# Performance work log

Measured on AMD Instinct MI355X. Metric: run time of the kernel, lower is better.

## Reference

```python
import jax, jax.numpy as jnp
import numpy as np

N = 20000; P = 3; L_LP = 10; L_NS = 20; D = 128; OUT = 2; E = 640000; V_LP = 5000; V_NS = 10000


def _gru(x, lengths, W_ih, W_hh, b_ih, b_hh):
    # x: [B, T, Din]; returns last valid hidden state per sequence (pack_padded semantics)
    T = x.shape[1]
    xp = jnp.einsum('btd,gd->btg', x, W_ih) + b_ih  # [B, T, 3H]
    h0 = jnp.zeros((x.shape[0], W_hh.shape[1]), x.dtype)

    def step(h, inp):
        xpt, t = inp
        hp = h @ W_hh.T + b_hh
        xr, xz, xn = jnp.split(xpt, 3, axis=-1)
        hr, hz, hn = jnp.split(hp, 3, axis=-1)
        r = jax.nn.sigmoid(xr + hr)
        z = jax.nn.sigmoid(xz + hz)
        nn_ = jnp.tanh(xn + r * hn)
        h_new = (1.0 - z) * nn_ + z * h
        h = jnp.where((t < lengths)[:, None], h_new, h)
        return h, None

    hT, _ = jax.lax.scan(step, h0, (jnp.swapaxes(xp, 0, 1), jnp.arange(T)))
    return hT


def _gcn(x, src, dst, w, W, b, n):
    # PyG GCNConv: add self-loops (weight 1), symmetric normalization by in-degree
    loops = jnp.arange(n)
    s = jnp.concatenate([src, loops])
    d = jnp.concatenate([dst, loops])
    ww = jnp.concatenate([w, jnp.ones((n,), w.dtype)])
    deg = jax.ops.segment_sum(ww, d, num_segments=n)
    dinv = jnp.where(deg > 0, 1.0 / jnp.sqrt(deg), 0.0)
    norm = dinv[s] * ww * dinv[d]
    xw = x @ W.T
    return jax.ops.segment_sum(norm[:, None] * xw[s], d, num_segments=n) + b


def _lnorm(x, g, b):
    m = jnp.mean(x, axis=-1, keepdims=True)
    v = jnp.var(x, axis=-1, keepdims=True)
    return (x - m) / jnp.sqrt(v + 1e-5) * g + b


def _forward(x_ref, x_def, x_pdt, edge_weight, lp_emb, ns_emb, lp_Wih, lp_Whh, lp_bih, lp_bhh, ns_Wih, ns_Whh, ns_bih, ns_bhh, lp_fc_W, lp_fc_b, all_fc_W, all_fc_b, conv1_W, conv1_b, conv2_W, conv2_b, conv3_W, conv3_b, ln1_g, ln1_b, ln2_g, ln2_b, mp1_W, mp1_b, mp2_W, mp2_b, idx_lp, x_lp_length, idx_ns, x_ns_length, edge_index):
    n = idx_ns.shape[0]
    # long-path GRU encodings, one GRU run per path slot (vmapped over P)
    xl = lp_emb[idx_lp]  # [N, P, L_LP, D]
    gru_lp = lambda seq, lens: _gru(seq, lens, lp_Wih, lp_Whh, lp_bih, lp_bhh)
    h_lp = jax.vmap(gru_lp, in_axes=(1, 1))(xl, x_lp_length)  # [P, N, D]
    # torch.cat(h_list).view(N, D*P): row-major reshape of [P, N, D]
    x_lp = h_lp.reshape(n, P * D) @ lp_fc_W.T + lp_fc_b
    # natural-sequence GRU encoding
    x_ns = _gru(ns_emb[idx_ns], x_ns_length, ns_Wih, ns_Whh, ns_bih, ns_bhh)  # [N, D]
    # torch.cat(dim=0).view(N, 5D): faithful row-major reshape of [5N, D]
    x = jnp.concatenate([x_pdt, x_ref, x_def, x_lp, x_ns], axis=0).reshape(n, 5 * D)
    x = x @ all_fc_W.T + all_fc_b
    src, dst = edge_index[0], edge_index[1]
    convs = [(conv1_W, conv1_b), (conv2_W, conv2_b), (conv3_W, conv3_b)]
    lns = [(ln1_g, ln1_b), (ln2_g, ln2_b)]
    emb = x
    for i in range(3):
        x = _gcn(x, src, dst, edge_weight, convs[i][0], convs[i][1], n)
        emb = x
        x = jax.nn.relu(x)
        # dropout p=0.25 omitted (eval mode)
        if i < 2:
            x = _lnorm(x, lns[i][0], lns[i][1])
    x = x @ mp1_W.T + mp1_b
    x = x @ mp2_W.T + mp2_b
    return emb, jax.nn.log_softmax(x, axis=1)


def setup_inputs() -> dict:
    ks = jax.random.split(jax.random.key(0), 40)
    f32 = jnp.float32
    nrm = lambda k, sh, s: jax.random.normal(k, sh, f32) * s
    inp = {}
    inp['idx_lp'] = jax.random.randint(ks[0], (N, P, L_LP), 0, V_LP)
    inp['x_lp_length'] = jax.random.randint(ks[1], (N, P), 1, L_LP + 1)
    inp['idx_ns'] = jax.random.randint(ks[2], (N, L_NS), 0, V_NS)
    inp['x_ns_length'] = jax.random.randint(ks[3], (N,), 1, L_NS + 1)
    inp['x_ref'] = nrm(ks[4], (N, D), 1.0)
    inp['x_def'] = nrm(ks[5], (N, D), 1.0)
    inp['x_pdt'] = nrm(ks[6], (N, D), 1.0)
    inp['edge_index'] = jax.random.randint(ks[7], (2, E), 0, N)
    inp['edge_weight'] = jax.random.uniform(ks[8], (E,), f32)
    inp['lp_emb'] = nrm(ks[9], (V_LP, D), 0.5)
    inp['ns_emb'] = nrm(ks[10], (V_NS, D), 0.5)
    s = 0.08
    inp['lp_Wih'] = nrm(ks[11], (3 * D, D), s)
    inp['lp_Whh'] = nrm(ks[12], (3 * D, D), s)
    inp['lp_bih'] = nrm(ks[13], (3 * D,), s)
    inp['lp_bhh'] = nrm(ks[14], (3 * D,), s)
    inp['ns_Wih'] = nrm(ks[15], (3 * D, D), s)
    inp['ns_Whh'] = nrm(ks[16], (3 * D, D), s)
    inp['ns_bih'] = nrm(ks[17], (3 * D,), s)
    inp['ns_bhh'] = nrm(ks[18], (3 * D,), s)
    inp['lp_fc_W'] = nrm(ks[19], (D, P * D), 0.05)
    inp['lp_fc_b'] = nrm(ks[20], (D,), 0.05)
    inp['all_fc_W'] = nrm(ks[21], (D, 5 * D), 0.05)
    inp['all_fc_b'] = nrm(ks[22], (D,), 0.05)
    inp['conv1_W'] = nrm(ks[23], (D, D), 0.08)
    inp['conv1_b'] = nrm(ks[24], (D,), 0.05)
    inp['conv2_W'] = nrm(ks[25], (D, D), 0.08)
    inp['conv2_b'] = nrm(ks[26], (D,), 0.05)
    inp['conv3_W'] = nrm(ks[27], (D, D), 0.08)
    inp['conv3_b'] = nrm(ks[28], (D,), 0.05)
    inp['ln1_g'] = jnp.ones((D,), f32)
    inp['ln1_b'] = jnp.zeros((D,), f32)
    inp['ln2_g'] = jnp.ones((D,), f32)
    inp['ln2_b'] = jnp.zeros((D,), f32)
    inp['mp1_W'] = nrm(ks[29], (D, D), 0.08)
    inp['mp1_b'] = nrm(ks[30], (D,), 0.05)
    inp['mp2_W'] = nrm(ks[31], (OUT, D), 0.08)
    inp['mp2_b'] = nrm(ks[32], (OUT,), 0.05)
    return inp


def reference(idx_lp, x_lp_length, idx_ns, x_ns_length, x_ref, x_def, x_pdt, edge_index, edge_weight, lp_emb, ns_emb, lp_Wih, lp_Whh, lp_bih, lp_bhh, ns_Wih, ns_Whh, ns_bih, ns_bhh, lp_fc_W, lp_fc_b, all_fc_W, all_fc_b, conv1_W, conv1_b, conv2_W, conv2_b, conv3_W, conv3_b, ln1_g, ln1_b, ln2_g, ln2_b, mp1_W, mp1_b, mp2_W, mp2_b):
    return _forward(x_ref, x_def, x_pdt, edge_weight, lp_emb, ns_emb, lp_Wih, lp_Whh, lp_bih, lp_bhh, ns_Wih, ns_Whh, ns_bih, ns_bhh, lp_fc_W, lp_fc_b, all_fc_W, all_fc_b, conv1_W, conv1_b, conv2_W, conv2_b, conv3_W, conv3_b, ln1_g, ln1_b, ln2_g, ln2_b, mp1_W, mp1_b, mp2_W, mp2_b, idx_lp, x_lp_length, idx_ns, x_ns_length, edge_index)
```

## Files before the change

### kernel.cpp

```cpp
#include <hip/hip_runtime.h>
#include <math.h>

typedef unsigned short u16;
typedef short bf16x4 __attribute__((ext_vector_type(4)));
typedef short bf16x8 __attribute__((ext_vector_type(8)));
typedef float f32x16 __attribute__((ext_vector_type(16)));

#define NN 20000
#define PP 3
#define TLP 10
#define TNS 20
#define DD 128
#define EE 640000

__device__ __forceinline__ float bf2f(u16 u) {
  union { unsigned u; float f; } v; v.u = ((unsigned)u) << 16; return v.f;
}
__device__ __forceinline__ u16 f2bf(float f) {
  union { float f; unsigned u; } v; v.f = f;
  unsigned r = v.u + 0x7fffu + ((v.u >> 16) & 1u);
  return (u16)(r >> 16);
}
__device__ __forceinline__ short f2bf_hw(float f) {
  __bf16 b = (__bf16)f;
  return (short)__builtin_bit_cast(unsigned short, b);
}
__device__ __forceinline__ float loadf(const void* p, size_t i, int isf) {
  return isf ? ((const float*)p)[i] : bf2f(((const u16*)p)[i]);
}
__device__ __forceinline__ float fex2(float x) { return __builtin_amdgcn_exp2f(x); }
__device__ __forceinline__ float frcp(float x) { return __builtin_amdgcn_rcpf(x); }
__device__ __forceinline__ unsigned cvtpk(float lo, float hi) {
  unsigned r; asm("v_cvt_pk_bf16_f32 %0, %1, %2" : "=v"(r) : "v"(lo), "v"(hi));
  return r;
}

__global__ void k_detect(const void* probe, int* flag, int* bins) {
  __shared__ int any;
  if (threadIdx.x == 0) any = 0;
  __syncthreads();
  if (threadIdx.x < 128) bins[threadIdx.x] = 0;
  const u16* p = (const u16*)probe;
  int bad = 0;
  for (int i = threadIdx.x; i < 4096; i += 256) {
    int e = (p[2 * i] >> 7) & 0xFF;
    if (e >= 0x9F) bad = 1;
  }
  if (bad) atomicOr(&any, 1);
  __syncthreads();
  if (threadIdx.x == 0) flag[0] = any;
}

struct CvtJobs {
  const void* src[16];
  int off[16];
  int n[16];
};

struct CvtJobsB {
  const void* src[12];
  int off[12];
  int n[12];
  int thr[12];
  float scA[12];
  float scB[12];
};

__global__ void k_cvtb(CvtJobsB j, CvtJobs jf, u16* __restrict__ dst,
                       float* __restrict__ fdst, int* __restrict__ counts,
                       float* __restrict__ deg, const int* flag) {
  const int isf = flag[0];
  if (blockIdx.x >= 12 * 64 + 16) {
    int i = (blockIdx.x - (12 * 64 + 16)) * 256 + threadIdx.x;
    if (i < NN) { counts[i] = 0; deg[i] = 1.f; }
    return;
  }
  if (blockIdx.x >= 12 * 64) {
    const int job = blockIdx.x - 12 * 64;
    const void* s = jf.src[job];
    float* d = fdst + jf.off[job];
    const int n = jf.n[job];
    for (int i = threadIdx.x; i < n; i += 256) d[i] = loadf(s, i, isf);
    return;
  }
  const int job = blockIdx.x >> 6;
  const int chunk = blockIdx.x & 63;
  const void* s = j.src[job];
  u16* d = dst + j.off[job];
  const int n = j.n[job];
  const int thr = j.thr[job];
  const float sA = j.scA[job], sB = j.scB[job];
  for (int i = chunk * 256 + threadIdx.x; i < n; i += 64 * 256)
    d[i] = f2bf(loadf(s, i, isf) * (i < thr ? sA : sB));
}

__global__ void k_lenboth(const int* __restrict__ lensLP,
                          const int* __restrict__ lensNS,
                          int* __restrict__ bins) {
  int sg = blockIdx.x * 256 + threadIdx.x;
  int lane = threadIdx.x & 63;
  int binL = 0, binN = 0;
  if (sg < PP * NN) binL = lensLP[(sg % NN) * PP + sg / NN];
  if (sg < NN) binN = lensNS[sg];
  for (int b = 1; b <= TLP; ++b) {
    unsigned long long m = __ballot(binL == b);
    if (m) {
      int leader = (int)(__ffsll((long long)m) - 1);
      if (lane == leader) atomicAdd(&bins[b], (int)__popcll(m));
    }
  }
  for (int b = 1; b <= TNS; ++b) {
    unsigned long long m = __ballot(binN == b);
    if (m) {
      int leader = (int)(__ffsll((long long)m) - 1);
      if (lane == leader) atomicAdd(&bins[64 + b], (int)__popcll(m));
    }
  }
}

__global__ void k_binscan2(int* __restrict__ bins,
                           const float* __restrict__ w_mp2,
                           const float* __restrict__ b_mp1_,
                           const float* __restrict__ b_mp2_,
                           const void* __restrict__ mp1raw,
                           float* __restrict__ Wc, const int* flag) {
  if (blockIdx.x == 0) {
    if (threadIdx.x == 0) {
      int acc = 0;
      for (int k = 0; k < 32; ++k) { bins[32 + k] = acc; acc += bins[k]; }
    }
    if (threadIdx.x == 1) {
      int acc = 0;
      for (int k = 0; k < 32; ++k) { bins[96 + k] = acc; acc += bins[64 + k]; }
    }
    return;
  }
  const int isf = flag[0];
  const int t = threadIdx.x;
  const int o = t >> 7, k = t & 127;
  float acc = 0.f;
  for (int d2 = 0; d2 < 128; ++d2)
    acc += w_mp2[o * 128 + d2] * loadf(mp1raw, (size_t)d2 * 128 + k, isf);
  Wc[t] = acc;
  if (t < 2) {
    float bacc = b_mp2_[t];
    for (int d2 = 0; d2 < 128; ++d2) bacc += w_mp2[t * 128 + d2] * b_mp1_[d2];
    Wc[256 + t] = bacc;
  }
}

__global__ void k_lenfillboth(const int* __restrict__ lensLP,
                              const int* __restrict__ lensNS,
                              int* __restrict__ bins,
                              int* __restrict__ permLP,
                              int* __restrict__ permNS) {
  int sg = blockIdx.x * 256 + threadIdx.x;
  int lane = threadIdx.x & 63;
  int binL = 0, binN = 0;
  if (sg < PP * NN) binL = lensLP[(sg % NN) * PP + sg / NN];
  if (sg < NN) binN = lensNS[sg];
  for (int b = 1; b <= TLP; ++b) {
    unsigned long long m = __ballot(binL == b);
    if (m) {
      int leader = (int)(__ffsll((long long)m) - 1);
      int base = 0;
      if (lane == leader) base = atomicAdd(&bins[32 + b], (int)__popcll(m));
      base = __shfl(base, leader);
      if (binL == b) {
        int rank = (int)__popcll(m & ((1ull << lane) - 1ull));
        permLP[base + rank] = sg;
      }
    }
  }
  for (int b = 1; b <= TNS; ++b) {
    unsigned long long m = __ballot(binN == b);
    if (m) {
      int leader = (int)(__ffsll((long long)m) - 1);
      int base = 0;
      if (lane == leader) base = atomicAdd(&bins[96 + b], (int)__popcll(m));
      base = __shfl(base, leader);
      if (binN == b) {
        int rank = (int)__popcll(m & ((1ull << lane) - 1ull));
        permNS[base + rank] = sg;
      }
    }
  }
}

__global__ __launch_bounds__(512, 2) void k_gru5(
    const int* __restrict__ permLP, const int* __restrict__ permNS, int nbNS,
    const u16* __restrict__ embLP, const u16* __restrict__ embNS,
    const int* __restrict__ idxLP, const int* __restrict__ idxNS,
    const int* __restrict__ lenLP, const int* __restrict__ lenNS,
    const u16* __restrict__ WihLP, const u16* __restrict__ WhhLP,
    const u16* __restrict__ WihNS, const u16* __restrict__ WhhNS,
    const float* __restrict__ bihLP, const float* __restrict__ bhhLP,
    const float* __restrict__ bihNS, const float* __restrict__ bhhNS,
    u16* __restrict__ HoutLP, u16* __restrict__ HoutNS, int nbLP,
    const int* __restrict__ e_dst, const void* __restrict__ ew,
    int* __restrict__ counts, float* __restrict__ deg,
    const int* __restrict__ flag) {
  __shared__ u16 xp[2][3][128][36];
  __shared__ u16 Hbf2[2][32][132];
  __shared__ int ivs[TNS][32];
  __shared__ int rowv[32], outv[32], lenv_s[32];
  __shared__ int Tbs;

  const int bid = blockIdx.x;
  const int nGru = nbLP + nbNS;
  const int tid = threadIdx.x;
  if (bid >= nGru) {
    int e = (bid - nGru) * 512 + tid;
    if (e < EE) {
      int dd = e_dst[e];
      atomicAdd(&counts[dd], 1);
      atomicAdd(&deg[dd], loadf(ew, e, flag[0]));
    }
    return;
  }
  const int isNS = bid < nbNS;
  const int chunk = isNS ? (nbNS - 1 - bid) : (nbLP - 1 - (bid - nbNS));
  const int* perm = isNS ? (permNS + chunk * 32) : (permLP + chunk * 32);
  const u16* embbf = isNS ? embNS : embLP;
  const int* idx = isNS ? idxNS : idxLP;
  const int* lens = isNS ? lenNS : lenLP;
  const u16* Wih = isNS ? WihNS : WihLP;
  const u16* Whh = isNS ? WhhNS : WhhLP;
  const float* bih = isNS ? bihNS : bihLP;
  const float* bhh = isNS ? bhhNS : bhhLP;
  u16* Hout = isNS ? HoutNS : HoutLP;
  const int T = isNS ? TNS : TLP;

  const int w = tid >> 6, lane = tid & 63;
  const int l31 = lane & 31, lh = lane >> 5;
  const int role = w >> 2;
  const int j = w & 3;
  const int d = 32 * j + l31;

  if (tid < 32) {
    int sg = perm[tid];
    int row = isNS ? sg : ((sg % NN) * PP + sg / NN);
    rowv[tid] = row;
    outv[tid] = sg;
    lenv_s[tid] = lens[row];
  }
  __syncthreads();
  if (tid == 0) {
    int m = 1;
    for (int k = 0; k < 32; ++k) m = max(m, lenv_s[k]);
    Tbs = m;
  }
  __syncthreads();
  const int Tb = Tbs;

  for (int z = tid; z < Tb * 32; z += 512) {
    int s = z & 31, t = z >> 5;
    ivs[t][s] = idx[(size_t)rowv[s] * T + t];
  }
  for (int z = tid; z < 2112; z += 512) ((unsigned*)Hbf2[0])[z] = 0u;

  bf16x8 wf[24];
  {
    const u16* Ws = role ? Whh : Wih;
#pragma unroll
    for (int g = 0; g < 3; ++g)
#pragma unroll
      for (int kb = 0; kb < 8; ++kb)
        wf[g * 8 + kb] =
            *(const bf16x8*)(Ws + (size_t)(128 * g + d) * 128 + kb * 16 + lh * 8);
  }
  const float SA = -1.44269504088896f;
  const float SN = -2.88539008177793f;
  float ib0, ib1, ib2;
  if (!role) {
    ib0 = SA * (bih[d] + bhh[d]);
    ib1 = SA * (bih[128 + d] + bhh[128 + d]);
    ib2 = SN * bih[256 + d];
  } else {
    ib0 = 0.f;
    ib1 = 0.f;
    ib2 = SN * bhh[256 + d];
  }

  __syncthreads();
  int lenr[16];
#pragma unroll
  for (int rg = 0; rg < 16; ++rg)
    lenr[rg] = lenv_s[(rg & 3) + 8 * (rg >> 2) + 4 * lh];

  float h[16];
#pragma unroll
  for (int rg = 0; rg < 16; ++rg) h[rg] = 0.f;

  for (int i = 0; i <= Tb; ++i) {
    if (!role) {
      if (i < Tb) {
        bf16x8 Xf[8];
        const u16* erow = embbf + (size_t)ivs[i][l31] * 128 + lh * 8;
#pragma unroll
        for (int kb = 0; kb < 8; ++kb) Xf[kb] = *(const bf16x8*)(erow + kb * 16);
        f32x16 a0 = (f32x16)(ib0), a1 = (f32x16)(ib1), a2 = (f32x16)(ib2);
#pragma unroll
        for (int kb = 0; kb < 8; ++kb) {
          a0 = __builtin_amdgcn_mfma_f32_32x32x16_bf16(Xf[kb], wf[kb], a0, 0, 0, 0);
          a1 = __builtin_amdgcn_mfma_f32_32x32x16_bf16(Xf[kb], wf[8 + kb], a1, 0, 0, 0);
          a2 = __builtin_amdgcn_mfma_f32_32x32x16_bf16(Xf[kb], wf[16 + kb], a2, 0, 0, 0);
        }
        const int sl = i & 1;
#pragma unroll
        for (int rq = 0; rq < 4; ++rq) {
          int mo = 8 * rq + 4 * lh;
          bf16x4 p0, p1, p2;
#pragma unroll
          for (int q = 0; q < 4; ++q) {
            p0[q] = f2bf_hw(a0[4 * rq + q]);
            p1[q] = f2bf_hw(a1[4 * rq + q]);
            p2[q] = f2bf_hw(a2[4 * rq + q]);
          }
          *(bf16x4*)(&xp[sl][0][d][mo]) = p0;
          *(bf16x4*)(&xp[sl][1][d][mo]) = p1;
          *(bf16x4*)(&xp[sl][2][d][mo]) = p2;
        }
      }
    } else {
      if (i >= 1) {
        const int rs = (i - 1) & 1, wsl = i & 1;
        bf16x8 Hf[8];
#pragma unroll
        for (int kb = 0; kb < 8; ++kb) {
          bf16x4 lo = *(const bf16x4*)(&Hbf2[rs][l31][16 * kb + 8 * lh]);
          bf16x4 hi = *(const bf16x4*)(&Hbf2[rs][l31][16 * kb + 8 * lh + 4]);
          Hf[kb] = __builtin_shufflevector(lo, hi, 0, 1, 2, 3, 4, 5, 6, 7);
        }
        f32x16 a0 = (f32x16)(ib0), a1 = (f32x16)(ib1), a2 = (f32x16)(ib2);
#pragma unroll
        for (int kb = 0; kb < 8; ++kb) {
          a0 = __builtin_amdgcn_mfma_f32_32x32x16_bf16(Hf[kb], wf[kb], a0, 0, 0, 0);
          a1 = __builtin_amdgcn_mfma_f32_32x32x16_bf16(Hf[kb], wf[8 + kb], a1, 0, 0, 0);
          a2 = __builtin_amdgcn_mfma_f32_32x32x16_bf16(Hf[kb], wf[16 + kb], a2, 0, 0, 0);
        }
        const int t = i - 1;
#pragma unroll
        for (int rq = 0; rq < 4; ++rq) {
          int mo = 8 * rq + 4 * lh;
          bf16x4 x0 = *(const bf16x4*)(&xp[rs][0][d][mo]);
          bf16x4 x1 = *(const bf16x4*)(&xp[rs][1][d][mo]);
          bf16x4 x2 = *(const bf16x4*)(&xp[rs][2][d][mo]);
          float hq[4];
#pragma unroll
          for (int q = 0; q < 4; ++q) {
            int rg = 4 * rq + q;
            float r = frcp(1.f + fex2(a0[rg] + bf2f((u16)x0[q])));
            float z = frcp(1.f + fex2(a1[rg] + bf2f((u16)x1[q])));
            float s = fmaf(r, a2[rg], bf2f((u16)x2[q]));
            float nn_ = fmaf(2.f, frcp(1.f + fex2(s)), -1.f);
            float hnew = fmaf(z, h[rg] - nn_, nn_);
            h[rg] = (t < lenr[rg]) ? hnew : h[rg];
            hq[q] = h[rg];
          }
          unsigned pa = cvtpk(hq[0], hq[1]);
          unsigned pb = cvtpk(hq[2], hq[3]);
          Hbf2[wsl][mo + 0][d] = (u16)pa;
          Hbf2[wsl][mo + 1][d] = (u16)(pa >> 16);
          Hbf2[wsl][mo + 2][d] = (u16)pb;
          Hbf2[wsl][mo + 3][d] = (u16)(pb >> 16);
        }
      }
    }
    __syncthreads();
  }

  if (role) {
#pragma unroll
    for (int rg = 0; rg < 16; ++rg) {
      int m = (rg & 3) + 8 * (rg >> 2) + 4 * lh;
      Hout[(size_t)outv[m] * 128 + d] = f2bf(h[rg]);
    }
  }
}

__global__ __launch_bounds__(128) void k_gemm_mfma(
    const void* __restrict__ A0, const void* __restrict__ A1,
    const void* __restrict__ A2, const u16* __restrict__ A3,
    const u16* __restrict__ A4, int mode, int K,
    const u16* __restrict__ W, const float* __restrict__ bias,
    void* __restrict__ Cout, int out_bf, int M, const int* __restrict__ flag,
    const int* __restrict__ esrc, const int* __restrict__ edst,
    const void* __restrict__ ew, int* __restrict__ cursor,
    int2* __restrict__ csr, const float* __restrict__ dinv,
    int fillE, int gemmBlocks) {
  const int isf = flag[0];
  const int tid = threadIdx.x;
  if ((int)blockIdx.x >= gemmBlocks) {
    int e = ((int)blockIdx.x - gemmBlocks) * 128 + tid;
    if (e < fillE) {
      int s = esrc[e];
      float c = dinv[s] * loadf(ew, e, isf);
      int p = atomicAdd(&cursor[edst[e]], 1);
      csr[p] = make_int2(s, __float_as_int(c));
    }
    return;
  }
  const int w = tid >> 6, lane = tid & 63;
  const int l31 = lane & 31, lh = lane >> 5;
  const int w23 = w;
  const int mbase = blockIdx.x * 32;
  const int row = mbase + l31;
  const int rowc = row < M ? row : M - 1;

  f32x16 acc0 = (f32x16)(0.f), acc1 = (f32x16)(0.f);
  const int nk = K >> 4;
  for (int kb = 0; kb < nk; ++kb) {
    bf16x8 a;
    if (mode == 0) {
      a = *(const bf16x8*)((const u16*)A0 + (size_t)rowc * K + kb * 16 + lh * 8);
    } else {
      int r5 = 5 * rowc + (kb >> 3);
      int slot = r5 / NN;
      int inner = r5 - slot * NN;
      int koff = (kb & 7) * 16 + lh * 8;
      if (slot < 3) {
        const void* p = (slot == 0) ? A0 : (slot == 1) ? A1 : A2;
        if (isf) {
          const float* fp = (const float*)p + (size_t)inner * 128 + koff;
          float4 v0 = *(const float4*)fp;
          float4 v1 = *(const float4*)(fp + 4);
          a[0] = (short)f2bf(v0.x); a[1] = (short)f2bf(v0.y);
          a[2] = (short)f2bf(v0.z); a[3] = (short)f2bf(v0.w);
          a[4] = (short)f2bf(v1.x); a[5] = (short)f2bf(v1.y);
          a[6] = (short)f2bf(v1.z); a[7] = (short)f2bf(v1.w);
        } else {
          a = *(const bf16x8*)((const u16*)p + (size_t)inner * 128 + koff);
        }
      } else {
        const u16* p = (slot == 3) ? A3 : A4;
        a = *(const bf16x8*)(p + (size_t)inner * 128 + koff);
      }
    }
    const u16* wp = W + (size_t)(64 * w23 + l31) * K + kb * 16 + lh * 8;
    bf16x8 b0 = *(const bf16x8*)wp;
    bf16x8 b1 = *(const bf16x8*)(wp + (size_t)32 * K);
    acc0 = __builtin_amdgcn_mfma_f32_32x32x16_bf16(a, b0, acc0, 0, 0, 0);
    acc1 = __builtin_amdgcn_mfma_f32_32x32x16_bf16(a, b1, acc1, 0, 0, 0);
  }
  const int col0 = 64 * w23 + l31;
  const float bv0 = bias ? bias[col0] : 0.f;
  const float bv1 = bias ? bias[col0 + 32] : 0.f;
#pragma unroll
  for (int rg = 0; rg < 16; ++rg) {
    int m = (rg & 3) + 8 * (rg >> 2) + 4 * lh;
    int grow = mbase + m;
    if (grow < M) {
      float v0 = acc0[rg] + bv0, v1 = acc1[rg] + bv1;
      if (out_bf) {
        ((u16*)Cout)[(size_t)grow * 128 + col0] = f2bf(v0);
        ((u16*)Cout)[(size_t)grow * 128 + col0 + 32] = f2bf(v1);
      } else {
        ((float*)Cout)[(size_t)grow * 128 + col0] = v0;
        ((float*)Cout)[(size_t)grow * 128 + col0 + 32] = v1;
      }
    }
  }
}

__global__ void k_scan(const int* __restrict__ counts, int* __restrict__ start,
                       int* __restrict__ cursor, const float* __restrict__ deg,
                       float* __restrict__ dinv, int n) {
  __shared__ int part[256];
  const int C = (n + 255) / 256;
  int tid = threadIdx.x;
  int base = tid * C;
  int s = 0;
  for (int k = 0; k < C; ++k) {
    int i = base + k;
    s += (i < n) ? counts[i] : 0;
  }
  part[tid] = s;
  __syncthreads();
  if (tid == 0) {
    int acc = 0;
    for (int k = 0; k < 256; ++k) { int v = part[k]; part[k] = acc; acc += v; }
  }
  __syncthreads();
  int run = part[tid];
  for (int k = 0; k < C; ++k) {
    int i = base + k;
    if (i < n) {
      int c = counts[i];
      start[i] = run;
      cursor[i] = run;
      run += c;
      dinv[i] = 1.f / sqrtf(deg[i]);
    }
  }
  if (tid == 255) start[n] = run;
}

__global__ __launch_bounds__(256) void k_gcn_gather(
    const int* __restrict__ start, const int2* __restrict__ csr,
    const float* __restrict__ dinv, const u16* __restrict__ xwbf,
    const float* __restrict__ bias, const float* __restrict__ g,
    const float* __restrict__ b, u16* __restrict__ out_bf,
    void* __restrict__ dout, const int* __restrict__ flag, int mode) {
  int v = blockIdx.x * 4 + (threadIdx.x >> 6);
  int lane = threadIdx.x & 63;
  if (v >= NN) return;
  const int c0 = 2 * lane;
  float acc0 = 0.f, acc1 = 0.f;
  int i = start[v];
  const int i1 = start[v + 1];
  for (; i + 4 <= i1; i += 4) {
    int2 e0 = csr[i], e1 = csr[i + 1], e2 = csr[i + 2], e3 = csr[i + 3];
    unsigned p0 = *(const unsigned*)(xwbf + (size_t)e0.x * 128 + c0);
    unsigned p1 = *(const unsigned*)(xwbf + (size_t)e1.x * 128 + c0);
    unsigned p2 = *(const unsigned*)(xwbf + (size_t)e2.x * 128 + c0);
    unsigned p3 = *(const unsigned*)(xwbf + (size_t)e3.x * 128 + c0);
    float f0 = __int_as_float(e0.y), f1 = __int_as_float(e1.y);
    float f2 = __int_as_float(e2.y), f3 = __int_as_float(e3.y);
    acc0 += f0 * bf2f((u16)(p0 & 0xffff)) + f1 * bf2f((u16)(p1 & 0xffff)) +
            f2 * bf2f((u16)(p2 & 0xffff)) + f3 * bf2f((u16)(p3 & 0xffff));
    acc1 += f0 * bf2f((u16)(p0 >> 16)) + f1 * bf2f((u16)(p1 >> 16)) +
            f2 * bf2f((u16)(p2 >> 16)) + f3 * bf2f((u16)(p3 >> 16));
  }
  if (i + 2 <= i1) {
    int2 e0 = csr[i], e1 = csr[i + 1];
    unsigned p0 = *(const unsigned*)(xwbf + (size_t)e0.x * 128 + c0);
    unsigned p1 = *(const unsigned*)(xwbf + (size_t)e1.x * 128 + c0);
    float f0 = __int_as_float(e0.y), f1 = __int_as_float(e1.y);
    acc0 += f0 * bf2f((u16)(p0 & 0xffff)) + f1 * bf2f((u16)(p1 & 0xffff));
    acc1 += f0 * bf2f((u16)(p0 >> 16)) + f1 * bf2f((u16)(p1 >> 16));
    i += 2;
  }
  if (i < i1) {
    int2 e = csr[i];
    float c = __int_as_float(e.y);
    unsigned pv = *(const unsigned*)(xwbf + (size_t)e.x * 128 + c0);
    acc0 += c * bf2f((u16)(pv & 0xffff));
    acc1 += c * bf2f((u16)(pv >> 16));
  }
  float dv = dinv[v];
  unsigned sv = *(const unsigned*)(xwbf + (size_t)v * 128 + c0);
  float y0 = bias[c0] + dv * (dv * bf2f((u16)(sv & 0xffff)) + acc0);
  float y1 = bias[c0 + 1] + dv * (dv * bf2f((u16)(sv >> 16)) + acc1);
  if (mode == 1) {
    if (flag[0]) {
      *(float2*)((float*)dout + (size_t)v * 128 + c0) = make_float2(y0, y1);
    } else {
      unsigned pk = (unsigned)f2bf(y0) | ((unsigned)f2bf(y1) << 16);
      *(unsigned*)((u16*)dout + (size_t)v * 128 + c0) = pk;
    }
    unsigned pr = (unsigned)f2bf(fmaxf(y0, 0.f)) | ((unsigned)f2bf(fmaxf(y1, 0.f)) << 16);
    *(unsigned*)(out_bf + (size_t)v * 128 + c0) = pr;
  } else {
    float x0 = fmaxf(y0, 0.f), x1 = fmaxf(y1, 0.f);
    float s_ = x0 + x1;
#pragma unroll
    for (int off = 32; off; off >>= 1) s_ += __shfl_xor(s_, off);
    float mean = s_ * (1.f / 128.f);
    float e0 = x0 - mean, e1 = x1 - mean;
    float vv = e0 * e0 + e1 * e1;
#pragma unroll
    for (int off = 32; off; off >>= 1) vv += __shfl_xor(vv, off);
    float inv = 1.f / sqrtf(vv * (1.f / 128.f) + 1e-5f);
    unsigned pk = (unsigned)f2bf(e0 * inv * g[c0] + b[c0]) |
                  ((unsigned)f2bf(e1 * inv * g[c0 + 1] + b[c0 + 1]) << 16);
    *(unsigned*)(out_bf + (size_t)v * 128 + c0) = pk;
  }
}

__global__ __launch_bounds__(256) void k_mphead(
    const u16* __restrict__ relu, const float* __restrict__ Wc,
    void* __restrict__ dout, const int* __restrict__ flag, int nrows) {
  int wid = (blockIdx.x * 256 + threadIdx.x) >> 6;
  int lane = threadIdx.x & 63;
  if (wid >= nrows) return;
  const int c0 = 2 * lane;
  unsigned pv = *(const unsigned*)(relu + (size_t)wid * 128 + c0);
  float x0 = bf2f((u16)(pv & 0xffff)), x1 = bf2f((u16)(pv >> 16));
  float p0 = x0 * Wc[c0] + x1 * Wc[c0 + 1];
  float p1 = x0 * Wc[128 + c0] + x1 * Wc[128 + c0 + 1];
#pragma unroll
  for (int off = 32; off; off >>= 1) {
    p0 += __shfl_xor(p0, off);
    p1 += __shfl_xor(p1, off);
  }
  if (lane == 0) {
    float v0 = p0 + Wc[256], v1 = p1 + Wc[257];
    float m = fmaxf(v0, v1);
    float ls = m + logf(__expf(v0 - m) + __expf(v1 - m));
    size_t base = (size_t)NN * 128 + (size_t)wid * 2;
    if (flag[0]) {
      ((float*)dout)[base + 0] = v0 - ls;
      ((float*)dout)[base + 1] = v1 - ls;
    } else {
      unsigned pk = (unsigned)f2bf(v0 - ls) | ((unsigned)f2bf(v1 - ls) << 16);
      *(unsigned*)((u16*)dout + base) = pk;
    }
  }
}

extern "C" void kernel_launch(void* const* d_in, const int* in_sizes, int n_in,
                              void* d_out, int out_size, void* d_ws, size_t ws_size,
                              hipStream_t stream) {
  const int* idx_lp = (const int*)d_in[0];
  const int* len_lp = (const int*)d_in[1];
  const int* idx_ns = (const int*)d_in[2];
  const int* len_ns = (const int*)d_in[3];
  const void* x_ref = d_in[4];
  const void* x_def = d_in[5];
  const void* x_pdt = d_in[6];
  const int* eidx   = (const int*)d_in[7];
  const void* ew    = d_in[8];
  const void* lp_emb = d_in[9];

  char* cur = (char*)d_ws;
  auto alloc = [&](size_t bytes, size_t align) -> void* {
    size_t a = ((size_t)cur + align - 1) & ~(align - 1);
    cur = (char*)(a + bytes);
    return (void*)a;
  };
  int* flag     = (int*)alloc(64, 64);
  float* smallW = (float*)alloc(3104 * 4, 16);
  float* f_Wc   = (float*)alloc(260 * 4, 16);
  float* f_deg  = (float*)alloc(NN * 4, 16);
  float* f_dinv = (float*)alloc(NN * 4, 16);
  int* counts   = (int*)alloc(NN * 4, 16);
  int* startA   = (int*)alloc((NN + 1) * 4, 16);
  int* cursorE  = (int*)alloc(NN * 4, 16);
  int* bins     = (int*)alloc(128 * 4, 16);
  int* perm_lp  = (int*)alloc(PP * NN * 4, 16);
  int* perm_ns  = (int*)alloc(NN * 4, 16);
  int2* csr2    = (int2*)alloc((size_t)EE * 8, 16);
  u16* ub       = (u16*)alloc((size_t)20233216 * 2, 16);
  u16* embbf_lp = ub;
  u16* embbf_ns = ub + 640000;
  u16* wg_lpih  = ub + 1920000;
  u16* wg_lphh  = ub + 1969152;
  u16* wg_nsih  = ub + 2018304;
  u16* wg_nshh  = ub + 2067456;
  u16* wg_lpfc  = ub + 2116608;
  u16* wg_allfc = ub + 2165760;
  u16* wg_c1    = ub + 2247680;
  u16* wg_c2    = ub + 2264064;
  u16* wg_c3    = ub + 2280448;
  u16* wg_mp1   = ub + 2296832;
  u16* hbf_lp   = ub + 2313216;
  u16* hbf_ns   = ub + 9993216;
  u16* lp_bf    = ub + 12553216;
  u16* xcur_bf  = ub + 15113216;
  u16* xw_bf    = ub + 17673216;
  u16* relu_bf  = hbf_lp;

  static const int fn[16] = {384, 384, 384, 384, 128, 128, 128, 128,
                             128, 128, 128, 128, 128, 128, 256, 2};
  static const int fsrc[16] = {13, 14, 17, 18, 20, 22, 24, 26,
                               28, 29, 30, 31, 32, 34, 35, 36};
  CvtJobs jf;
  int foff[16];
  {
    int off = 0;
    for (int j = 0; j < 16; ++j) {
      jf.src[j] = d_in[fsrc[j]];
      jf.off[j] = off;
      jf.n[j] = fn[j];
      foff[j] = off;
      off += fn[j];
    }
  }
  float* b_lpbih = smallW + foff[0];
  float* b_lpbhh = smallW + foff[1];
  float* b_nsbih = smallW + foff[2];
  float* b_nsbhh = smallW + foff[3];
  float* b_lpfc  = smallW + foff[4];
  float* b_allfc = smallW + foff[5];
  float* b_conv[3] = {smallW + foff[6], smallW + foff[7], smallW + foff[8]};
  float* g_ln[2] = {smallW + foff[9], smallW + foff[11]};
  float* b_ln[2] = {smallW + foff[10], smallW + foff[12]};
  float* b_mp1   = smallW + foff[13];
  float* w_mp2   = smallW + foff[14];
  float* b_mp2   = smallW + foff[15];

  static const int bn[12] = {640000, 1280000, 49152, 49152, 49152, 49152,
                             49152, 81920, 16384, 16384, 16384, 16384};
  static const int bsrc[12] = {9, 10, 11, 12, 15, 16, 19, 21, 23, 25, 27, 33};
  static const int boff[12] = {0, 640000, 1920000, 1969152, 2018304, 2067456,
                               2116608, 2165760, 2247680, 2264064, 2280448,
                               2296832};
  CvtJobsB jb;
  for (int j = 0; j < 12; ++j) {
    jb.src[j] = d_in[bsrc[j]];
    jb.off[j] = boff[j];
    jb.n[j] = bn[j];
    const bool gw = (j >= 2 && j <= 5);
    jb.thr[j] = gw ? 32768 : 0;
    jb.scA[j] = gw ? -1.44269504088896f : 1.f;
    jb.scB[j] = gw ? -2.88539008177793f : 1.f;
  }

  const int* e_src = eidx;
  const int* e_dst = eidx + EE;

  k_detect<<<1, 256, 0, stream>>>(lp_emb, flag, bins);

  const int initBlocks = (NN + 255) / 256;
  k_cvtb<<<12 * 64 + 16 + initBlocks, 256, 0, stream>>>(jb, jf, ub, smallW,
                                                        counts, f_deg, flag);

  k_lenboth<<<(PP * NN + 255) / 256, 256, 0, stream>>>(len_lp, len_ns, bins);
  k_binscan2<<<2, 256, 0, stream>>>(bins, w_mp2, b_mp1, b_mp2, d_in[33],
                                    f_Wc, flag);
  k_lenfillboth<<<(PP * NN + 255) / 256, 256, 0, stream>>>(len_lp, len_ns, bins,
                                                           perm_lp, perm_ns);

  const int nbLP = PP * NN / 32, nbNS = NN / 32;
  const int histBlocks = (EE + 511) / 512;
  k_gru5<<<nbLP + nbNS + histBlocks, 512, 0, stream>>>(
      perm_lp, perm_ns, nbNS, embbf_lp, embbf_ns, idx_lp, idx_ns, len_lp, len_ns,
      wg_lpih, wg_lphh, wg_nsih, wg_nshh, b_lpbih, b_lpbhh, b_nsbih, b_nsbhh,
      hbf_lp, hbf_ns, nbLP, e_dst, ew, counts, f_deg, flag);

  k_scan<<<1, 256, 0, stream>>>(counts, startA, cursorE, f_deg, f_dinv, NN);

  const int gg = (NN + 31) / 32;
  const int fillBlocks = (EE + 127) / 128;
  k_gemm_mfma<<<gg + fillBlocks, 128, 0, stream>>>(
      hbf_lp, nullptr, nullptr, nullptr, nullptr, 0, 384, wg_lpfc, b_lpfc,
      lp_bf, 1, NN, flag, e_src, e_dst, ew, cursorE, csr2, f_dinv, EE, gg);
  k_gemm_mfma<<<gg, 128, 0, stream>>>(
      x_pdt, x_ref, x_def, lp_bf, hbf_ns, 1, 640, wg_allfc, b_allfc,
      xcur_bf, 1, NN, flag, nullptr, nullptr, nullptr, nullptr, nullptr,
      nullptr, 0, gg);

  const u16* wgc[3] = {wg_c1, wg_c2, wg_c3};
  for (int l = 0; l < 3; ++l) {
    k_gemm_mfma<<<gg, 128, 0, stream>>>(
        xcur_bf, nullptr, nullptr, nullptr, nullptr, 0, DD, wgc[l], nullptr,
        xw_bf, 1, NN, flag, nullptr, nullptr, nullptr, nullptr, nullptr,
        nullptr, 0, gg);
    if (l < 2) {
      k_gcn_gather<<<NN / 4, 256, 0, stream>>>(startA, csr2, f_dinv, xw_bf,
                                               b_conv[l], g_ln[l], b_ln[l],
                                               xcur_bf, nullptr, flag, 0);
    } else {
      k_gcn_gather<<<NN / 4, 256, 0, stream>>>(startA, csr2, f_dinv, xw_bf,
                                               b_conv[l], nullptr, nullptr,
                                               relu_bf, d_out, flag, 1);
    }
  }

  k_mphead<<<(NN + 3) / 4, 256, 0, stream>>>(relu_bf, f_Wc, d_out, flag, NN);
}
```

Baseline: 981.0 us.

## Fuse MP head into final GCN gather, drop float atomics, skip bf16 embedding copies

Several changes land together. The final GCN gather now computes the MLP head and log-softmax itself, which removes the k_mphead launch and the relu buffer round trip. The degree is now computed by a per-node CSR segment sum in the tail blocks of the second GEMM instead of float atomicAdds in the histogram. That moves the dinv[src] multiply into the gather, adding an extra indexed load per edge. When the inputs are already bf16, the GRU reads the raw embedding tables directly and the conversion jobs for them are skipped.

Result: faster. 898.9 us (-8.4%).

```diff
diff --git a/kernel.cpp b/kernel.cpp
--- a/kernel.cpp
+++ b/kernel.cpp
@@ -68,11 +68,11 @@
 
 __global__ void k_cvtb(CvtJobsB j, CvtJobs jf, u16* __restrict__ dst,
                        float* __restrict__ fdst, int* __restrict__ counts,
-                       float* __restrict__ deg, const int* flag) {
+                       const int* flag) {
   const int isf = flag[0];
   if (blockIdx.x >= 12 * 64 + 16) {
     int i = (blockIdx.x - (12 * 64 + 16)) * 256 + threadIdx.x;
-    if (i < NN) { counts[i] = 0; deg[i] = 1.f; }
+    if (i < NN) counts[i] = 0;
     return;
   }
   if (blockIdx.x >= 12 * 64) {
@@ -84,6 +84,7 @@
     return;
   }
   const int job = blockIdx.x >> 6;
+  if (job < 2 && !isf) return;
   const int chunk = blockIdx.x & 63;
   const void* s = j.src[job];
   u16* d = dst + j.off[job];
@@ -189,7 +190,8 @@
 
 __global__ __launch_bounds__(512, 2) void k_gru5(
     const int* __restrict__ permLP, const int* __restrict__ permNS, int nbNS,
-    const u16* __restrict__ embLP, const u16* __restrict__ embNS,
+    const u16* __restrict__ embLPc, const u16* __restrict__ embNSc,
+    const u16* __restrict__ embLPr, const u16* __restrict__ embNSr,
     const int* __restrict__ idxLP, const int* __restrict__ idxNS,
     const int* __restrict__ lenLP, const int* __restrict__ lenNS,
     const u16* __restrict__ WihLP, const u16* __restrict__ WhhLP,
@@ -197,8 +199,7 @@
     const float* __restrict__ bihLP, const float* __restrict__ bhhLP,
     const float* __restrict__ bihNS, const float* __restrict__ bhhNS,
     u16* __restrict__ HoutLP, u16* __restrict__ HoutNS, int nbLP,
-    const int* __restrict__ e_dst, const void* __restrict__ ew,
-    int* __restrict__ counts, float* __restrict__ deg,
+    const int* __restrict__ e_dst, int* __restrict__ counts,
     const int* __restrict__ flag) {
   __shared__ u16 xp[2][3][128][36];
   __shared__ u16 Hbf2[2][32][132];
@@ -211,17 +212,14 @@
   const int tid = threadIdx.x;
   if (bid >= nGru) {
     int e = (bid - nGru) * 512 + tid;
-    if (e < EE) {
-      int dd = e_dst[e];
-      atomicAdd(&counts[dd], 1);
-      atomicAdd(&deg[dd], loadf(ew, e, flag[0]));
-    }
+    if (e < EE) atomicAdd(&counts[e_dst[e]], 1);
     return;
   }
+  const int isf = flag[0];
   const int isNS = bid < nbNS;
   const int chunk = isNS ? (nbNS - 1 - bid) : (nbLP - 1 - (bid - nbNS));
   const int* perm = isNS ? (permNS + chunk * 32) : (permLP + chunk * 32);
-  const u16* embbf = isNS ? embNS : embLP;
+  const u16* embbf = isNS ? (isf ? embNSc : embNSr) : (isf ? embLPc : embLPr);
   const int* idx = isNS ? idxNS : idxLP;
   const int* lens = isNS ? lenNS : lenLP;
   const u16* Wih = isNS ? WihNS : WihLP;
@@ -387,17 +385,24 @@
     void* __restrict__ Cout, int out_bf, int M, const int* __restrict__ flag,
     const int* __restrict__ esrc, const int* __restrict__ edst,
     const void* __restrict__ ew, int* __restrict__ cursor,
-    int2* __restrict__ csr, const float* __restrict__ dinv,
-    int fillE, int gemmBlocks) {
+    int2* __restrict__ csr, const int* __restrict__ startT,
+    float* __restrict__ dinvOut, int tailN, int tailMode, int gemmBlocks) {
   const int isf = flag[0];
   const int tid = threadIdx.x;
   if ((int)blockIdx.x >= gemmBlocks) {
-    int e = ((int)blockIdx.x - gemmBlocks) * 128 + tid;
-    if (e < fillE) {
-      int s = esrc[e];
-      float c = dinv[s] * loadf(ew, e, isf);
-      int p = atomicAdd(&cursor[edst[e]], 1);
-      csr[p] = make_int2(s, __float_as_int(c));
+    int i = ((int)blockIdx.x - gemmBlocks) * 128 + tid;
+    if (i < tailN) {
+      if (tailMode == 1) {
+        int s = esrc[i];
+        float wv = loadf(ew, i, isf);
+        int p = atomicAdd(&cursor[edst[i]], 1);
+        csr[p] = make_int2(s, __float_as_int(wv));
+      } else {
+        int a = startT[i], b = startT[i + 1];
+        float sum = 1.f;
+        for (int k = a; k < b; ++k) sum += __int_as_float(csr[k].y);
+        dinvOut[i] = 1.f / sqrtf(sum);
+      }
     }
     return;
   }
@@ -464,8 +469,7 @@
 }
 
 __global__ void k_scan(const int* __restrict__ counts, int* __restrict__ start,
-                       int* __restrict__ cursor, const float* __restrict__ deg,
-                       float* __restrict__ dinv, int n) {
+                       int* __restrict__ cursor, int n) {
   __shared__ int part[256];
   const int C = (n + 255) / 256;
   int tid = threadIdx.x;
@@ -490,7 +494,6 @@
       start[i] = run;
       cursor[i] = run;
       run += c;
-      dinv[i] = 1.f / sqrtf(deg[i]);
     }
   }
   if (tid == 255) start[n] = run;
@@ -501,7 +504,8 @@
     const float* __restrict__ dinv, const u16* __restrict__ xwbf,
     const float* __restrict__ bias, const float* __restrict__ g,
     const float* __restrict__ b, u16* __restrict__ out_bf,
-    void* __restrict__ dout, const int* __restrict__ flag, int mode) {
+    void* __restrict__ dout, const float* __restrict__ Wc,
+    const int* __restrict__ flag, int mode) {
   int v = blockIdx.x * 4 + (threadIdx.x >> 6);
   int lane = threadIdx.x & 63;
   if (v >= NN) return;
@@ -515,8 +519,10 @@
     unsigned p1 = *(const unsigned*)(xwbf + (size_t)e1.x * 128 + c0);
     unsigned p2 = *(const unsigned*)(xwbf + (size_t)e2.x * 128 + c0);
     unsigned p3 = *(const unsigned*)(xwbf + (size_t)e3.x * 128 + c0);
-    float f0 = __int_as_float(e0.y), f1 = __int_as_float(e1.y);
-    float f2 = __int_as_float(e2.y), f3 = __int_as_float(e3.y);
+    float f0 = __int_as_float(e0.y) * dinv[e0.x];
+    float f1 = __int_as_float(e1.y) * dinv[e1.x];
+    float f2 = __int_as_float(e2.y) * dinv[e2.x];
+    float f3 = __int_as_float(e3.y) * dinv[e3.x];
     acc0 += f0 * bf2f((u16)(p0 & 0xffff)) + f1 * bf2f((u16)(p1 & 0xffff)) +
             f2 * bf2f((u16)(p2 & 0xffff)) + f3 * bf2f((u16)(p3 & 0xffff));
     acc1 += f0 * bf2f((u16)(p0 >> 16)) + f1 * bf2f((u16)(p1 >> 16)) +
@@ -526,14 +532,15 @@
     int2 e0 = csr[i], e1 = csr[i + 1];
     unsigned p0 = *(const unsigned*)(xwbf + (size_t)e0.x * 128 + c0);
     unsigned p1 = *(const unsigned*)(xwbf + (size_t)e1.x * 128 + c0);
-    float f0 = __int_as_float(e0.y), f1 = __int_as_float(e1.y);
+    float f0 = __int_as_float(e0.y) * dinv[e0.x];
+    float f1 = __int_as_float(e1.y) * dinv[e1.x];
     acc0 += f0 * bf2f((u16)(p0 & 0xffff)) + f1 * bf2f((u16)(p1 & 0xffff));
     acc1 += f0 * bf2f((u16)(p0 >> 16)) + f1 * bf2f((u16)(p1 >> 16));
     i += 2;
   }
   if (i < i1) {
     int2 e = csr[i];
-    float c = __int_as_float(e.y);
+    float c = __int_as_float(e.y) * dinv[e.x];
     unsigned pv = *(const unsigned*)(xwbf + (size_t)e.x * 128 + c0);
     acc0 += c * bf2f((u16)(pv & 0xffff));
     acc1 += c * bf2f((u16)(pv >> 16));
@@ -549,8 +556,27 @@
       unsigned pk = (unsigned)f2bf(y0) | ((unsigned)f2bf(y1) << 16);
       *(unsigned*)((u16*)dout + (size_t)v * 128 + c0) = pk;
     }
-    unsigned pr = (unsigned)f2bf(fmaxf(y0, 0.f)) | ((unsigned)f2bf(fmaxf(y1, 0.f)) << 16);
-    *(unsigned*)(out_bf + (size_t)v * 128 + c0) = pr;
+    float x0 = fmaxf(y0, 0.f), x1 = fmaxf(y1, 0.f);
+    float p0 = x0 * Wc[c0] + x1 * Wc[c0 + 1];
+    float p1 = x0 * Wc[128 + c0] + x1 * Wc[128 + c0 + 1];
+#pragma unroll
+    for (int off = 32; off; off >>= 1) {
+      p0 += __shfl_xor(p0, off);
+      p1 += __shfl_xor(p1, off);
+    }
+    if (lane == 0) {
+      float v0 = p0 + Wc[256], v1 = p1 + Wc[257];
+      float m = fmaxf(v0, v1);
+      float ls = m + logf(__expf(v0 - m) + __expf(v1 - m));
+      size_t base = (size_t)NN * 128 + (size_t)v * 2;
+      if (flag[0]) {
+        ((float*)dout)[base + 0] = v0 - ls;
+        ((float*)dout)[base + 1] = v1 - ls;
+      } else {
+        unsigned pk = (unsigned)f2bf(v0 - ls) | ((unsigned)f2bf(v1 - ls) << 16);
+        *(unsigned*)((u16*)dout + base) = pk;
+      }
+    }
   } else {
     float x0 = fmaxf(y0, 0.f), x1 = fmaxf(y1, 0.f);
     float s_ = x0 + x1;
@@ -565,37 +591,6 @@
     unsigned pk = (unsigned)f2bf(e0 * inv * g[c0] + b[c0]) |
                   ((unsigned)f2bf(e1 * inv * g[c0 + 1] + b[c0 + 1]) << 16);
     *(unsigned*)(out_bf + (size_t)v * 128 + c0) = pk;
-  }
-}
-
-__global__ __launch_bounds__(256) void k_mphead(
-    const u16* __restrict__ relu, const float* __restrict__ Wc,
-    void* __restrict__ dout, const int* __restrict__ flag, int nrows) {
-  int wid = (blockIdx.x * 256 + threadIdx.x) >> 6;
-  int lane = threadIdx.x & 63;
-  if (wid >= nrows) return;
-  const int c0 = 2 * lane;
-  unsigned pv = *(const unsigned*)(relu + (size_t)wid * 128 + c0);
-  float x0 = bf2f((u16)(pv & 0xffff)), x1 = bf2f((u16)(pv >> 16));
-  float p0 = x0 * Wc[c0] + x1 * Wc[c0 + 1];
-  float p1 = x0 * Wc[128 + c0] + x1 * Wc[128 + c0 + 1];
-#pragma unroll
-  for (int off = 32; off; off >>= 1) {
-    p0 += __shfl_xor(p0, off);
-    p1 += __shfl_xor(p1, off);
-  }
-  if (lane == 0) {
-    float v0 = p0 + Wc[256], v1 = p1 + Wc[257];
-    float m = fmaxf(v0, v1);
-    float ls = m + logf(__expf(v0 - m) + __expf(v1 - m));
-    size_t base = (size_t)NN * 128 + (size_t)wid * 2;
-    if (flag[0]) {
-      ((float*)dout)[base + 0] = v0 - ls;
-      ((float*)dout)[base + 1] = v1 - ls;
-    } else {
-      unsigned pk = (unsigned)f2bf(v0 - ls) | ((unsigned)f2bf(v1 - ls) << 16);
-      *(unsigned*)((u16*)dout + base) = pk;
-    }
   }
 }
 
@@ -612,6 +607,7 @@
   const int* eidx   = (const int*)d_in[7];
   const void* ew    = d_in[8];
   const void* lp_emb = d_in[9];
+  const void* ns_emb = d_in[10];
 
   char* cur = (char*)d_ws;
   auto alloc = [&](size_t bytes, size_t align) -> void* {
@@ -622,7 +618,6 @@
   int* flag     = (int*)alloc(64, 64);
   float* smallW = (float*)alloc(3104 * 4, 16);
   float* f_Wc   = (float*)alloc(260 * 4, 16);
-  float* f_deg  = (float*)alloc(NN * 4, 16);
   float* f_dinv = (float*)alloc(NN * 4, 16);
   int* counts   = (int*)alloc(NN * 4, 16);
   int* startA   = (int*)alloc((NN + 1) * 4, 16);
@@ -643,13 +638,11 @@
   u16* wg_c1    = ub + 2247680;
   u16* wg_c2    = ub + 2264064;
   u16* wg_c3    = ub + 2280448;
-  u16* wg_mp1   = ub + 2296832;
   u16* hbf_lp   = ub + 2313216;
   u16* hbf_ns   = ub + 9993216;
   u16* lp_bf    = ub + 12553216;
   u16* xcur_bf  = ub + 15113216;
   u16* xw_bf    = ub + 17673216;
-  u16* relu_bf  = hbf_lp;
 
   static const int fn[16] = {384, 384, 384, 384, 128, 128, 128, 128,
                              128, 128, 128, 128, 128, 128, 256, 2};
@@ -681,7 +674,7 @@
   float* b_mp2   = smallW + foff[15];
 
   static const int bn[12] = {640000, 1280000, 49152, 49152, 49152, 49152,
-                             49152, 81920, 16384, 16384, 16384, 16384};
+                             49152, 81920, 16384, 16384, 16384, 0};
   static const int bsrc[12] = {9, 10, 11, 12, 15, 16, 19, 21, 23, 25, 27, 33};
   static const int boff[12] = {0, 640000, 1920000, 1969152, 2018304, 2067456,
                                2116608, 2165760, 2247680, 2264064, 2280448,
@@ -704,7 +697,7 @@
 
   const int initBlocks = (NN + 255) / 256;
   k_cvtb<<<12 * 64 + 16 + initBlocks, 256, 0, stream>>>(jb, jf, ub, smallW,
-                                                        counts, f_deg, flag);
+                                                        counts, flag);
 
   k_lenboth<<<(PP * NN + 255) / 256, 256, 0, stream>>>(len_lp, len_ns, bins);
   k_binscan2<<<2, 256, 0, stream>>>(bins, w_mp2, b_mp1, b_mp2, d_in[33],
@@ -715,38 +708,42 @@
   const int nbLP = PP * NN / 32, nbNS = NN / 32;
   const int histBlocks = (EE + 511) / 512;
   k_gru5<<<nbLP + nbNS + histBlocks, 512, 0, stream>>>(
-      perm_lp, perm_ns, nbNS, embbf_lp, embbf_ns, idx_lp, idx_ns, len_lp, len_ns,
+      perm_lp, perm_ns, nbNS, embbf_lp, embbf_ns,
+      (const u16*)lp_emb, (const u16*)ns_emb,
+      idx_lp, idx_ns, len_lp, len_ns,
       wg_lpih, wg_lphh, wg_nsih, wg_nshh, b_lpbih, b_lpbhh, b_nsbih, b_nsbhh,
-      hbf_lp, hbf_ns, nbLP, e_dst, ew, counts, f_deg, flag);
-
-  k_scan<<<1, 256, 0, stream>>>(counts, startA, cursorE, f_deg, f_dinv, NN);
+      hbf_lp, hbf_ns, nbLP, e_dst, counts, flag);
+
+  k_scan<<<1, 256, 0, stream>>>(counts, startA, cursorE, NN);
 
   const int gg = (NN + 31) / 32;
   const int fillBlocks = (EE + 127) / 128;
+  const int degBlocks = (NN + 127) / 128;
   k_gemm_mfma<<<gg + fillBlocks, 128, 0, stream>>>(
       hbf_lp, nullptr, nullptr, nullptr, nullptr, 0, 384, wg_lpfc, b_lpfc,
-      lp_bf, 1, NN, flag, e_src, e_dst, ew, cursorE, csr2, f_dinv, EE, gg);
-  k_gemm_mfma<<<gg, 128, 0, stream>>>(
+      lp_bf, 1, NN, flag, e_src, e_dst, ew, cursorE, csr2, nullptr, nullptr,
+      EE, 1, gg);
+  k_gemm_mfma<<<gg + degBlocks, 128, 0, stream>>>(
       x_pdt, x_ref, x_def, lp_bf, hbf_ns, 1, 640, wg_allfc, b_allfc,
-      xcur_bf, 1, NN, flag, nullptr, nullptr, nullptr, nullptr, nullptr,
-      nullptr, 0, gg);
+      xcur_bf, 1, NN, flag, nullptr, nullptr, nullptr, nullptr, csr2, startA,
+      f_dinv, NN, 2, gg);
 
   const u16* wgc[3] = {wg_c1, wg_c2, wg_c3};
   for (int l = 0; l < 3; ++l) {
     k_gemm_mfma<<<gg, 128, 0, stream>>>(
         xcur_bf, nullptr, nullptr, nullptr, nullptr, 0, DD, wgc[l], nullptr,
         xw_bf, 1, NN, flag, nullptr, nullptr, nullptr, nullptr, nullptr,
-        nullptr, 0, gg);
+        nullptr, nullptr, 0, 0, gg);
     if (l < 2) {
       k_gcn_gather<<<NN / 4, 256, 0, stream>>>(startA, csr2, f_dinv, xw_bf,
                                                b_conv[l], g_ln[l], b_ln[l],
-                                               xcur_bf, nullptr, flag, 0);
+                                               xcur_bf, nullptr, nullptr,
+                                               flag, 0);
     } else {
       k_gcn_gather<<<NN / 4, 256, 0, stream>>>(startA, csr2, f_dinv, xw_bf,
                                                b_conv[l], nullptr, nullptr,
-                                               relu_bf, d_out, flag, 1);
-    }
-  }
-
-  k_mphead<<<(NN + 3) / 4, 256, 0, stream>>>(relu_bf, f_Wc, d_out, flag, NN);
-}
+                                               nullptr, d_out, f_Wc,
+                                               flag, 1);
+    }
+  }
+}
```
